# Optimization experiments

Measured on AMD Instinct MI355X. Metric: run time of the kernel, lower is better.

Reference implementation:

```python
import jax, jax.numpy as jnp
import numpy as np


def setup_inputs() -> dict:
    key = jax.random.key(0)
    k1, k2 = jax.random.split(key)
    B, C, H, W = 16, 32, 32, 32
    NUM = 32
    x = jax.random.normal(k1, (B, C, H, W), dtype=jnp.float32)
    # torch init: (rand(num, depth, 9) - 0.5) * 1
    neighbors = jax.random.uniform(k2, (NUM, C, 9), dtype=jnp.float32) - 0.5
    return {"x": x, "neighbors": neighbors}


def reference(x, neighbors):
    """ConvNearestNeightbor forward.

    For each of the 9 zero-padded 3x3 shifts of x, compute |x_shift - neighbor|
    broadcast over the `num` codebook axis, and take the elementwise max over
    the 9 shifts. Equivalent to the torch code's max over dim=3 of the
    (B, num, C, 9, H, W) abs-diff tensor, but computed incrementally so the
    9-axis intermediate is never materialized.
    """
    B, C, H, W = x.shape
    num = neighbors.shape[0]
    xp = jnp.pad(x, ((0, 0), (0, 0), (1, 1), (1, 1)))  # zero borders
    out = None
    k = 0
    for row in (-1, 0, 1):
        for col in (-1, 0, 1):
            # y[b,c,k,i,j] = x[b,c,i-row,j-col] (0 outside) == padded slice
            xs = xp[:, :, 1 - row:1 - row + H, 1 - col:1 - col + W]  # (B,C,H,W)
            nb = neighbors[:, :, k]                                  # (num,C)
            d = jnp.abs(xs[:, None] - nb[None, :, :, None, None])    # (B,num,C,H,W)
            out = d if out is None else jnp.maximum(out, d)
            k += 1
    return out.reshape(B, num * C, H, W)
```

## Files before the change

kernel.cpp:

```cpp
#include <hip/hip_runtime.h>


#define BB 16
#define CC 32
#define HH 32
#define WW 32
#define NUMN 32

__global__ __launch_bounds__(256) void conv_nn_kernel(
    const float* __restrict__ x,
    const float* __restrict__ neighbors,
    float* __restrict__ out)
{
    __shared__ float tile[HH + 2][WW + 4];
    __shared__ float nlds[NUMN * 9];

    const int bc = blockIdx.x;
    const int b  = bc >> 5;
    const int c  = bc & 31;
    const int t  = threadIdx.x;

    const float* xplane = x + (b * CC + c) * (HH * WW);
    for (int idx = t; idx < 34 * 34; idx += 256) {
        int row = idx / 34;
        int col = idx - row * 34;
        int h = row - 1, w = col - 1;
        float v = 0.0f;
        if ((unsigned)h < (unsigned)HH && (unsigned)w < (unsigned)WW)
            v = xplane[h * WW + w];
        tile[row][col] = v;
    }
    for (int i = t; i < NUMN * 9; i += 256) {
        int n = i / 9;
        int k = i - n * 9;
        nlds[i] = neighbors[(n * CC + c) * 9 + k];
    }
    __syncthreads();

    const int h  = t >> 3;
    const int w0 = (t & 7) * 4;

    float xr[3][6];
    #pragma unroll
    for (int r = 0; r < 3; ++r)
        #pragma unroll
        for (int cc2 = 0; cc2 < 6; ++cc2)
            xr[r][cc2] = tile[h + r][w0 + cc2];

    float* oplane = out + (size_t)((b * NUMN) * CC + c) * (HH * WW) + t * 4;
    const int nstride = CC * HH * WW;

    #pragma unroll 2
    for (int n = 0; n < NUMN; ++n) {
        float nb[9];
        #pragma unroll
        for (int k = 0; k < 9; ++k) nb[k] = nlds[n * 9 + k];

        float acc0 = -1.0f, acc1 = -1.0f, acc2 = -1.0f, acc3 = -1.0f;
        #pragma unroll
        for (int rr = 0; rr < 3; ++rr) {
            #pragma unroll
            for (int cc2 = 0; cc2 < 3; ++cc2) {
                const float nv = nb[rr * 3 + cc2];
                acc0 = fmaxf(acc0, fabsf(xr[2 - rr][0 + 2 - cc2] - nv));
                acc1 = fmaxf(acc1, fabsf(xr[2 - rr][1 + 2 - cc2] - nv));
                acc2 = fmaxf(acc2, fabsf(xr[2 - rr][2 + 2 - cc2] - nv));
                acc3 = fmaxf(acc3, fabsf(xr[2 - rr][3 + 2 - cc2] - nv));
            }
        }
        float4 v = make_float4(acc0, acc1, acc2, acc3);
        *reinterpret_cast<float4*>(oplane + (size_t)n * nstride) = v;
    }
}

extern "C" void kernel_launch(void* const* d_in, const int* in_sizes, int n_in,
                              void* d_out, int out_size, void* d_ws, size_t ws_size,
                              hipStream_t stream) {
    const float* x         = (const float*)d_in[0];
    const float* neighbors = (const float*)d_in[1];
    float* out             = (float*)d_out;

    dim3 grid(BB * CC);
    dim3 block(256);
    conv_nn_kernel<<<grid, block, 0, stream>>>(x, neighbors, out);
}
```

Baseline: 94.04 us.

## Split neighbor axis across grid.y blocks and use nontemporal output stores

The grid gains a second dimension so each block handles 4 of the 32 codebook entries instead of all 32. The grid grows from 512 to 4096 blocks, which gives more parallelism for the write-bound output. Output stores become nontemporal vector stores, the max chain is seeded with the first difference, and neighbor loading is simplified. The cost is that each block reloads the input plane tile, multiplying input reads and halo-staging work by 8.

```diff
diff --git a/kernel.cpp b/kernel.cpp
--- a/kernel.cpp
+++ b/kernel.cpp
@@ -6,6 +6,9 @@
 #define HH 32
 #define WW 32
 #define NUMN 32
+#define NPB 4
+
+typedef float f32x4 __attribute__((ext_vector_type(4)));
 
 __global__ __launch_bounds__(256) void conv_nn_kernel(
     const float* __restrict__ x,
@@ -13,11 +16,12 @@
     float* __restrict__ out)
 {
     __shared__ float tile[HH + 2][WW + 4];
-    __shared__ float nlds[NUMN * 9];
+    __shared__ float nlds[NPB * 9];
 
     const int bc = blockIdx.x;
     const int b  = bc >> 5;
     const int c  = bc & 31;
+    const int n0 = blockIdx.y * NPB;
     const int t  = threadIdx.x;
 
     const float* xplane = x + (b * CC + c) * (HH * WW);
@@ -30,10 +34,10 @@
             v = xplane[h * WW + w];
         tile[row][col] = v;
     }
-    for (int i = t; i < NUMN * 9; i += 256) {
-        int n = i / 9;
-        int k = i - n * 9;
-        nlds[i] = neighbors[(n * CC + c) * 9 + k];
+    if (t < NPB * 9) {
+        int n = t / 9;
+        int k = t - n * 9;
+        nlds[t] = neighbors[((n0 + n) * CC + c) * 9 + k];
     }
     __syncthreads();
 
@@ -44,32 +48,35 @@
     #pragma unroll
     for (int r = 0; r < 3; ++r)
         #pragma unroll
-        for (int cc2 = 0; cc2 < 6; ++cc2)
-            xr[r][cc2] = tile[h + r][w0 + cc2];
+        for (int j = 0; j < 6; ++j)
+            xr[r][j] = tile[h + r][w0 + j];
 
-    float* oplane = out + (size_t)((b * NUMN) * CC + c) * (HH * WW) + t * 4;
+    float* oplane = out + (size_t)((b * NUMN + n0) * CC + c) * (HH * WW) + t * 4;
     const int nstride = CC * HH * WW;
 
-    #pragma unroll 2
-    for (int n = 0; n < NUMN; ++n) {
+    #pragma unroll
+    for (int ni = 0; ni < NPB; ++ni) {
         float nb[9];
         #pragma unroll
-        for (int k = 0; k < 9; ++k) nb[k] = nlds[n * 9 + k];
+        for (int k = 0; k < 9; ++k) nb[k] = nlds[ni * 9 + k];
 
-        float acc0 = -1.0f, acc1 = -1.0f, acc2 = -1.0f, acc3 = -1.0f;
+        float acc0 = fabsf(xr[2][2] - nb[0]);
+        float acc1 = fabsf(xr[2][3] - nb[0]);
+        float acc2 = fabsf(xr[2][4] - nb[0]);
+        float acc3 = fabsf(xr[2][5] - nb[0]);
         #pragma unroll
-        for (int rr = 0; rr < 3; ++rr) {
-            #pragma unroll
-            for (int cc2 = 0; cc2 < 3; ++cc2) {
-                const float nv = nb[rr * 3 + cc2];
-                acc0 = fmaxf(acc0, fabsf(xr[2 - rr][0 + 2 - cc2] - nv));
-                acc1 = fmaxf(acc1, fabsf(xr[2 - rr][1 + 2 - cc2] - nv));
-                acc2 = fmaxf(acc2, fabsf(xr[2 - rr][2 + 2 - cc2] - nv));
-                acc3 = fmaxf(acc3, fabsf(xr[2 - rr][3 + 2 - cc2] - nv));
-            }
+        for (int kk = 1; kk < 9; ++kk) {
+            const int rr  = kk / 3;
+            const int cc2 = kk - rr * 3;
+            const float nv = nb[kk];
+            acc0 = fmaxf(acc0, fabsf(xr[2 - rr][0 + 2 - cc2] - nv));
+            acc1 = fmaxf(acc1, fabsf(xr[2 - rr][1 + 2 - cc2] - nv));
+            acc2 = fmaxf(acc2, fabsf(xr[2 - rr][2 + 2 - cc2] - nv));
+            acc3 = fmaxf(acc3, fabsf(xr[2 - rr][3 + 2 - cc2] - nv));
         }
-        float4 v = make_float4(acc0, acc1, acc2, acc3);
-        *reinterpret_cast<float4*>(oplane + (size_t)n * nstride) = v;
+        f32x4 v = { acc0, acc1, acc2, acc3 };
+        __builtin_nontemporal_store(v,
+            reinterpret_cast<f32x4*>(oplane + (size_t)ni * nstride));
     }
 }
 
@@ -80,7 +87,7 @@
     const float* neighbors = (const float*)d_in[1];
     float* out             = (float*)d_out;
 
-    dim3 grid(BB * CC);
+    dim3 grid(BB * CC, NUMN / NPB);
     dim3 block(256);
     conv_nn_kernel<<<grid, block, 0, stream>>>(x, neighbors, out);
 }
```

Result: faster. 85.52 us (-9.1%).
